# Performance work log

Hardware: AMD Instinct MI355X
Metric: run time of the kernel (lower is better)

## Reference

```python
import jax, jax.numpy as jnp
import numpy as np

B, C, T = 256, 9, 128
D, S, NL, EXP, DTR, DCONV = 24, 16, 4, 2, 2, 4
DI = EXP * D  # 48
STEMK, PK, PS = 5, 16, 4
NP = (T - PK) // PS + 1  # 29 patches
NCLS = 6


def setup_inputs() -> dict:
    key = jax.random.key(0)
    ks = iter(jax.random.split(key, 48))
    r = lambda shape, s=0.02: jax.random.normal(next(ks), shape, jnp.float32) * s
    return dict(
        x=jax.random.normal(next(ks), (B, T, C), jnp.float32),
        stem_w=r((D, 1, STEMK), 0.4),
        stem_bn_g=jnp.ones((D,)), stem_bn_b=jnp.zeros((D,)),
        stem_bn_m=jnp.zeros((D,)), stem_bn_v=jnp.ones((D,)),
        pd_w=r((D, 1, PK), 0.3),
        pp_w=r((D, D, 1), 0.3),
        patch_bn_g=jnp.ones((D,)), patch_bn_b=jnp.zeros((D,)),
        patch_bn_m=jnp.zeros((D,)), patch_bn_v=jnp.ones((D,)),
        pos_embed=r((1, NP, D)),
        ln1_g=jnp.ones((NL, D)), ln1_b=jnp.zeros((NL, D)),
        ln2_g=jnp.ones((NL, D)), ln2_b=jnp.zeros((NL, D)),
        in_w=r((NL, 2 * DI, D), 0.05),
        conv_w=r((NL, DI, 1, DCONV), 0.3), conv_b=jnp.zeros((NL, DI)),
        xproj_w=r((NL, DTR + 2 * S, DI), 0.05),
        dt_w=r((NL, DI, DTR), 0.1), dt_b=jnp.full((NL, DI), -2.0),
        A_log=jnp.log(jnp.broadcast_to(jnp.arange(1, S + 1, dtype=jnp.float32), (NL, DI, S))),
        Dp=jnp.ones((NL, DI)),
        out_w=r((NL, D, DI), 0.05),
        attn_w=r((D, D)), attn_b=jnp.zeros((D,)),
        ctx=r((D,)),
        head_g=jnp.ones((D,)), head_b=jnp.zeros((D,)),
        head_w=r((NCLS, D)), head_bias=jnp.zeros((NCLS,)),
    )


def _conv1d(x, w, stride, pad, groups=1):
    # x: [N, Cin, L], w: [Cout, Cin//groups, K]
    return jax.lax.conv_general_dilated(
        x, w, (stride,), [pad], dimension_numbers=('NCH', 'OIH', 'NCH'),
        feature_group_count=groups)


def _bn(x, g, b, m, v):  # eval-mode BatchNorm1d on [N, C, L]
    return (x - m[:, None]) * jax.lax.rsqrt(v[:, None] + 1e-5) * g[:, None] + b[:, None]


def _ln(x, g, b):
    mu = x.mean(-1, keepdims=True)
    var = ((x - mu) ** 2).mean(-1, keepdims=True)
    return (x - mu) * jax.lax.rsqrt(var + 1e-5) * g + b


def _selective_scan(u, dt, A, Bm, Cm):
    # u, dt: [N,L,DI]; A: [DI,S]; Bm, Cm: [N,L,S]
    dA = jnp.exp(dt[..., None] * A)                      # [N,L,DI,S]
    dBu = (dt * u)[..., None] * Bm[:, :, None, :]        # [N,L,DI,S]

    def step(h, inp):
        dA_t, dBu_t, C_t = inp
        h = dA_t * h + dBu_t                             # [N,DI,S]
        y = jnp.einsum('nds,ns->nd', h, C_t)
        return h, y

    h0 = jnp.zeros(dA.shape[:1] + dA.shape[2:], dA.dtype)
    _, ys = jax.lax.scan(step, h0, (dA.swapaxes(0, 1), dBu.swapaxes(0, 1), Cm.swapaxes(0, 1)))
    return ys.swapaxes(0, 1)                             # [N,L,DI]


def _mamba(x, in_w, conv_w, conv_b, xproj_w, dt_w, dt_b, A_log, Dp, out_w):
    # x: [N,L,D]
    xz = x @ in_w.T                                      # [N,L,2*DI]
    u, z = jnp.split(xz, 2, axis=-1)
    # causal depthwise conv (torch pads d_conv-1 both sides then truncates to L)
    uc = _conv1d(u.swapaxes(1, 2), conv_w, 1, (DCONV - 1, 0), groups=DI)
    uc = jax.nn.silu(uc + conv_b[None, :, None]).swapaxes(1, 2)   # [N,L,DI]
    dbl = uc @ xproj_w.T                                 # [N,L,DTR+2S]
    dtr, Bm, Cm = jnp.split(dbl, [DTR, DTR + S], axis=-1)
    dt = jax.nn.softplus(dtr @ dt_w.T + dt_b)            # [N,L,DI]
    A = -jnp.exp(A_log)                                  # [DI,S]
    y = _selective_scan(uc, dt, A, Bm, Cm) + uc * Dp
    y = y * jax.nn.silu(z)
    return y @ out_w.T                                   # [N,L,D]


def reference(x, stem_w, stem_bn_g, stem_bn_b, stem_bn_m, stem_bn_v,
              pd_w, pp_w, patch_bn_g, patch_bn_b, patch_bn_m, patch_bn_v,
              pos_embed, ln1_g, ln1_b, ln2_g, ln2_b,
              in_w, conv_w, conv_b, xproj_w, dt_w, dt_b, A_log, Dp, out_w,
              attn_w, attn_b, ctx, head_g, head_b, head_w, head_bias):
    Bsz = x.shape[0]
    # channel-independent reshape: [B,T,C] -> [B*C,1,T]
    h = x.transpose(0, 2, 1).reshape(Bsz * C, 1, T)
    # CI stem: shared single-channel conv + BN + SiLU
    h = _conv1d(h, stem_w, 1, (STEMK // 2, STEMK // 2))
    h = jax.nn.silu(_bn(h, stem_bn_g, stem_bn_b, stem_bn_m, stem_bn_v))  # [N,D,T]
    # patch embed: depthwise conv (k=16,s=4,pad=4,groups=D) + pointwise + BN
    h = _conv1d(h, pd_w, PS, (PK // 4, PK // 4), groups=D)
    h = _conv1d(h, pp_w, 1, (0, 0))
    h = _bn(h, patch_bn_g, patch_bn_b, patch_bn_m, patch_bn_v)
    h = h.swapaxes(1, 2)[:, :NP, :] + pos_embed          # [N,NP,D]
    # weight-tied bidirectional Mamba blocks
    for i in range(NL):
        res = h
        hn = _ln(h, ln1_g[i], ln1_b[i])
        args = (in_w[i], conv_w[i], conv_b[i], xproj_w[i], dt_w[i], dt_b[i], A_log[i], Dp[i], out_w[i])
        fwd = _mamba(hn, *args)
        bwd = jnp.flip(_mamba(jnp.flip(hn, axis=1), *args), axis=1)
        h = _ln(res + fwd + bwd, ln2_g[i], ln2_b[i])
    # gated temporal attention pooling
    u = jnp.tanh(h @ attn_w.T + attn_b)                  # [N,NP,D]
    alpha = jax.nn.softmax(jnp.einsum('nld,d->nl', u, ctx), axis=-1)
    c = jnp.einsum('nl,nld->nd', alpha, h)               # [N,D]
    # channel fusion: mean over sensor channels
    c = c.reshape(Bsz, C, D).mean(axis=1)                # [B,D]
    # head
    c = _ln(c, head_g, head_b)
    return c @ head_w.T + head_bias                      # [B,NCLS]
```

## Files before the change

### kernel.cpp

```cpp
#include <hip/hip_runtime.h>
#include <hip/hip_bf16.h>
#include <math.h>

#define B_    256
#define C_    9
#define T_    128
#define D_    24
#define S_    16
#define NL_   4
#define DI_   48
#define NP_   29
#define NSEQ  (B_ * C_)
#define NCLS_ 6

#define LOG2E 1.44269504088896f

#if __has_builtin(__builtin_amdgcn_exp2f)
#define EXP2F __builtin_amdgcn_exp2f
#else
#define EXP2F exp2f
#endif

__device__ __forceinline__ float fsilu(float x) {
    return __fdividef(x, 1.f + __expf(-x));
}

struct Params {
    const float *x;
    const float *stem_w, *stem_bn_g, *stem_bn_b, *stem_bn_m, *stem_bn_v;
    const float *pd_w, *pp_w, *patch_bn_g, *patch_bn_b, *patch_bn_m, *patch_bn_v;
    const float *pos_embed, *ln1_g, *ln1_b, *ln2_g, *ln2_b;
    const float *in_w, *conv_w, *conv_b, *xproj_w, *dt_w, *dt_b, *A_log, *Dp, *out_w;
    const float *attn_w, *attn_b, *ctx;
    float *cout;
};

__device__ __forceinline__ void ln_rows(const float* src, float* dst,
                                        const float* g, const float* bb, int tid) {
    int row = tid >> 3, sub = tid & 7;
    if (row < NP_) {
        const float* r = src + row * 24;
        float s = 0.f;
        for (int j = sub; j < 24; j += 8) s += r[j];
        s += __shfl_xor(s, 1); s += __shfl_xor(s, 2); s += __shfl_xor(s, 4);
        float mu = s * (1.f / 24.f);
        float v = 0.f;
        for (int j = sub; j < 24; j += 8) { float d0 = r[j] - mu; v = fmaf(d0, d0, v); }
        v += __shfl_xor(v, 1); v += __shfl_xor(v, 2); v += __shfl_xor(v, 4);
        float rs = rsqrtf(v * (1.f / 24.f) + 1e-5f);
        for (int j = sub; j < 24; j += 8) dst[row * 24 + j] = (r[j] - mu) * rs * g[j] + bb[j];
    }
}

#define OF_H    0
#define OF_HN   696
#define OF_U    1392
#define OF_Z    2784
#define OF_UCF  4176
#define OF_UCB  5568
#define OF_BCF  6960
#define OF_BCB  7888
#define OF_DTRF 8816
#define OF_DTRB 8874
#define SM_TOT  8932

__global__ __launch_bounds__(256, 4) void mamba_seq_kernel(Params P) {
    __shared__ float sm[SM_TOT];
    const int tid = threadIdx.x;
    const int n = blockIdx.x;
    const int b = n / C_, cch = n - b * C_;

    float* s_h    = sm + OF_H;
    float* s_hn   = sm + OF_HN;
    float* s_u    = sm + OF_U;
    float* s_z    = sm + OF_Z;
    float* s_ucf  = sm + OF_UCF;
    float* s_ucb  = sm + OF_UCB;
    float* s_bcf  = sm + OF_BCF;
    float* s_bcb  = sm + OF_BCB;
    float* s_dtrf = sm + OF_DTRF;
    float* s_dtrb = sm + OF_DTRB;

    float* xp  = sm + OF_UCF;
    float* h0p = sm + OF_UCF + 132;

    if (tid < 132) {
        float v = 0.f;
        int t = tid - 2;
        if (t >= 0 && t < T_) v = P.x[(b * T_ + t) * C_ + cch];
        xp[tid] = v;
    }
    for (int idx = tid; idx < 24 * 8; idx += 256) {
        int d = idx >> 3, j = idx & 7;
        h0p[d * 136 + (j < 4 ? j : j + 128)] = 0.f;
    }
    __syncthreads();
    for (int idx = tid; idx < 24 * 128; idx += 256) {
        int d = idx >> 7, t = idx & 127;
        const float* w = P.stem_w + d * 5;
        float acc = 0.f;
        #pragma unroll
        for (int k = 0; k < 5; k++) acc = fmaf(w[k], xp[t + k], acc);
        float sc = rsqrtf(P.stem_bn_v[d] + 1e-5f) * P.stem_bn_g[d];
        float val = (acc - P.stem_bn_m[d]) * sc + P.stem_bn_b[d];
        h0p[d * 136 + 4 + t] = fsilu(val);
    }
    __syncthreads();
    for (int idx = tid; idx < 24 * 31; idx += 256) {
        int d = idx / 31, l = idx - d * 31;
        const float* w = P.pd_w + d * 16;
        const float* src = h0p + d * 136 + l * 4;
        float acc = 0.f;
        #pragma unroll
        for (int k = 0; k < 16; k++) acc = fmaf(w[k], src[k], acc);
        s_u[idx] = acc;
    }
    __syncthreads();
    for (int idx = tid; idx < NP_ * 24; idx += 256) {
        int l = idx / 24, e = idx - l * 24;
        const float* w = P.pp_w + e * 24;
        float acc = 0.f;
        #pragma unroll
        for (int d = 0; d < 24; d++) acc = fmaf(w[d], s_u[d * 31 + l], acc);
        float sc = rsqrtf(P.patch_bn_v[e] + 1e-5f) * P.patch_bn_g[e];
        acc = (acc - P.patch_bn_m[e]) * sc + P.patch_bn_b[e];
        s_h[idx] = acc + P.pos_embed[idx];
    }
    __syncthreads();

    for (int il = 0; il < NL_; ++il) {
        const float* in_w_i   = P.in_w   + il * 96 * 24;
        const float* conv_w_i = P.conv_w + il * 48 * 4;
        const float* conv_b_i = P.conv_b + il * 48;
        const float* xpr_i    = P.xproj_w+ il * 34 * 48;
        const float* dt_w_i   = P.dt_w   + il * 48 * 2;
        const float* dt_b_i   = P.dt_b   + il * 48;
        const float* A_log_i  = P.A_log  + il * 48 * 16;
        const float* Dp_i     = P.Dp     + il * 48;
        const float* out_w_i  = P.out_w  + il * 24 * 48;

        ln_rows(s_h, s_hn, P.ln1_g + il * 24, P.ln1_b + il * 24, tid);
        __syncthreads();

        if (tid < 192) {
            int j  = tid >> 1;
            int l0 = (tid & 1) ? 15 : 0;
            int l1 = (tid & 1) ? NP_ : 15;
            const float4* w4 = (const float4*)(in_w_i + j * 24);
            float4 w0 = w4[0], w1 = w4[1], w2 = w4[2], w3 = w4[3], w4v = w4[4], w5 = w4[5];
            float* dst = (j < 48) ? (s_u + j) : (s_z + (j - 48));
            for (int l = l0; l < l1; ++l) {
                const float4* h4 = (const float4*)(s_hn + l * 24);
                float4 a0 = h4[0], a1 = h4[1], a2 = h4[2], a3 = h4[3], a4 = h4[4], a5 = h4[5];
                float acc;
                acc = a0.x * w0.x; acc = fmaf(a0.y, w0.y, acc); acc = fmaf(a0.z, w0.z, acc); acc = fmaf(a0.w, w0.w, acc);
                acc = fmaf(a1.x, w1.x, acc); acc = fmaf(a1.y, w1.y, acc); acc = fmaf(a1.z, w1.z, acc); acc = fmaf(a1.w, w1.w, acc);
                acc = fmaf(a2.x, w2.x, acc); acc = fmaf(a2.y, w2.y, acc); acc = fmaf(a2.z, w2.z, acc); acc = fmaf(a2.w, w2.w, acc);
                acc = fmaf(a3.x, w3.x, acc); acc = fmaf(a3.y, w3.y, acc); acc = fmaf(a3.z, w3.z, acc); acc = fmaf(a3.w, w3.w, acc);
                acc = fmaf(a4.x, w4v.x, acc); acc = fmaf(a4.y, w4v.y, acc); acc = fmaf(a4.z, w4v.z, acc); acc = fmaf(a4.w, w4v.w, acc);
                acc = fmaf(a5.x, w5.x, acc); acc = fmaf(a5.y, w5.y, acc); acc = fmaf(a5.z, w5.z, acc); acc = fmaf(a5.w, w5.w, acc);
                dst[l * 48] = acc;
            }
        }
        __syncthreads();

        for (int idx = tid; idx < NP_ * 48; idx += 256) {
            int l = idx / 48, d = idx - l * 48;
            const float* w = conv_w_i + d * 4;
            float w0 = w[0], w1 = w[1], w2 = w[2], w3 = w[3];
            float bb = conv_b_i[d];
            float accf = bb, accb = bb;
            if (l >= 3) accf = fmaf(w0, s_u[(l - 3) * 48 + d], accf);
            if (l >= 2) accf = fmaf(w1, s_u[(l - 2) * 48 + d], accf);
            if (l >= 1) accf = fmaf(w2, s_u[(l - 1) * 48 + d], accf);
            accf = fmaf(w3, s_u[l * 48 + d], accf);
            if (l + 3 < NP_) accb = fmaf(w0, s_u[(l + 3) * 48 + d], accb);
            if (l + 2 < NP_) accb = fmaf(w1, s_u[(l + 2) * 48 + d], accb);
            if (l + 1 < NP_) accb = fmaf(w2, s_u[(l + 1) * 48 + d], accb);
            accb = fmaf(w3, s_u[l * 48 + d], accb);
            s_ucf[idx] = fsilu(accf);
            s_ucb[idx] = fsilu(accb);
            s_z[idx] = fsilu(s_z[idx]);
        }
        __syncthreads();

        if (tid < 204) {
            int lg = tid / 68;
            int ch = tid - lg * 68;
            int l0 = lg * 10;
            int l1 = (lg == 2) ? NP_ : (l0 + 10);
            int dir = ch >= 34;
            int j = ch - (dir ? 34 : 0);
            const float* ucp = dir ? s_ucb : s_ucf;
            const float4* w4 = (const float4*)(xpr_i + j * 48);
            float4 w[12];
            #pragma unroll
            for (int q = 0; q < 12; q++) w[q] = w4[q];
            float* dst; int stride;
            if (j < 2) { dst = (dir ? s_dtrb : s_dtrf) + j; stride = 2; }
            else       { dst = (dir ? s_bcb  : s_bcf ) + (j - 2); stride = 32; }
            for (int l = l0; l < l1; ++l) {
                const float4* u4 = (const float4*)(ucp + l * 48);
                float acc = 0.f;
                #pragma unroll
                for (int q = 0; q < 12; q++) {
                    float4 a = u4[q];
                    acc = fmaf(a.x, w[q].x, fmaf(a.y, w[q].y, fmaf(a.z, w[q].z, fmaf(a.w, w[q].w, acc))));
                }
                dst[l * stride] = acc;
            }
        }
        __syncthreads();

        {
            int wv = tid >> 6, lane = tid & 63;
            if (wv < 2 && lane < 48) {
                const int d = lane;
                const float* dtr = wv ? s_dtrb : s_dtrf;
                float* ucio      = wv ? s_ucb  : s_ucf;
                const float* bc  = wv ? s_bcb  : s_bcf;
                float dtw0 = dt_w_i[d * 2], dtw1 = dt_w_i[d * 2 + 1], dtb = dt_b_i[d];
                float Dpd = Dp_i[d];
                float A2[16];
                bool alin = true;
                {
                    const float4* a4 = (const float4*)(A_log_i + d * 16);
                    #pragma unroll
                    for (int q = 0; q < 4; q++) {
                        float4 av = a4[q];
                        A2[4*q+0] = -__expf(av.x) * LOG2E;
                        A2[4*q+1] = -__expf(av.y) * LOG2E;
                        A2[4*q+2] = -__expf(av.z) * LOG2E;
                        A2[4*q+3] = -__expf(av.w) * LOG2E;
                    }
                    float a0c = A2[0];
                    #pragma unroll
                    for (int s = 1; s < 16; s++)
                        alin = alin && (fabsf(A2[s] - (s + 1) * a0c) <= 1e-4f * (s + 1) * fabsf(a0c));
                }
                float hs[16];
                #pragma unroll
                for (int s = 0; s < 16; s++) hs[s] = 0.f;

                if (alin) {
                    const float a0 = A2[0];
                    int l = wv ? (NP_ - 1) : 0;
                    float2 tt = *(const float2*)(dtr + l * 2);
                    float u_ld = ucio[l * 48 + d];
                    float draw = fmaf(tt.y, dtw1, fmaf(tt.x, dtw0, dtb));
                    float dtc = (draw > 15.f) ? draw : __logf(1.f + __expf(draw));
                    float dtu = dtc * u_ld;
                    float r1 = EXP2F(dtc * a0);
                    float r2 = r1 * r1, r4 = r2 * r2, r8 = r4 * r4;

                    for (int p = 0; p < NP_; p++) {
                        const int lc = l;
                        const float u_c = u_ld, dtu_c = dtu;
                        const float c1 = r1, c2 = r2, c4 = r4, c8 = r8;
                        if (p + 1 < NP_) {
                            l = wv ? (NP_ - 2 - p) : (p + 1);
                            tt = *(const float2*)(dtr + l * 2);
                            u_ld = ucio[l * 48 + d];
                            draw = fmaf(tt.y, dtw1, fmaf(tt.x, dtw0, dtb));
                            dtc = (draw > 15.f) ? draw : __logf(1.f + __expf(draw));
                            dtu = dtc * u_ld;
                            r1 = EXP2F(dtc * a0);
                            r2 = r1 * r1; r4 = r2 * r2; r8 = r4 * r4;
                        }
                        const float4* bcv = (const float4*)(bc + lc * 32);
                        float4 B0 = bcv[0], B1 = bcv[1], B2 = bcv[2], B3 = bcv[3];
                        float4 C0 = bcv[4], C1 = bcv[5], C2 = bcv[6], C3 = bcv[7];
                        float p3  = c2 * c1,  p5  = c4 * c1,  p6  = c4 * c2,  p7  = c4 * p3;
                        float p9  = c8 * c1,  p10 = c8 * c2,  p11 = c8 * p3,  p12 = c8 * c4;
                        float p13 = c8 * p5,  p14 = c8 * p6,  p15 = c8 * p7,  p16 = c8 * c8;
                        float y0 = 0.f, y1 = 0.f, y2 = 0.f, y3 = 0.f;
#define SFX(si, dA, Bc, Cc, ya) { hs[si] = fmaf(dA, hs[si], dtu_c * (Bc)); ya = fmaf(hs[si], (Cc), ya); }
                        SFX(0,  c1,  B0.x, C0.x, y0) SFX(1,  c2,  B0.y, C0.y, y1)
                        SFX(2,  p3,  B0.z, C0.z, y2) SFX(3,  c4,  B0.w, C0.w, y3)
                        SFX(4,  p5,  B1.x, C1.x, y0) SFX(5,  p6,  B1.y, C1.y, y1)
                        SFX(6,  p7,  B1.z, C1.z, y2) SFX(7,  c8,  B1.w, C1.w, y3)
                        SFX(8,  p9,  B2.x, C2.x, y0) SFX(9,  p10, B2.y, C2.y, y1)
                        SFX(10, p11, B2.z, C2.z, y2) SFX(11, p12, B2.w, C2.w, y3)
                        SFX(12, p13, B3.x, C3.x, y0) SFX(13, p14, B3.y, C3.y, y1)
                        SFX(14, p15, B3.z, C3.z, y2) SFX(15, p16, B3.w, C3.w, y3)
#undef SFX
                        float y = (y0 + y1) + (y2 + y3);
                        float v = fmaf(u_c, Dpd, y) * s_z[lc * 48 + d];
                        ucio[lc * 48 + d] = v;
                    }
                } else {
                    for (int p = 0; p < NP_; p++) {
                        int l = wv ? (NP_ - 1 - p) : p;
                        float2 tt = *(const float2*)(dtr + l * 2);
                        float draw = fmaf(tt.y, dtw1, fmaf(tt.x, dtw0, dtb));
                        float dtc = (draw > 15.f) ? draw : __logf(1.f + __expf(draw));
                        float u_ld = ucio[l * 48 + d];
                        float dtu = dtc * u_ld;
                        const float4* bcv = (const float4*)(bc + l * 32);
                        float4 B0 = bcv[0], B1 = bcv[1], B2 = bcv[2], B3 = bcv[3];
                        float4 C0 = bcv[4], C1 = bcv[5], C2 = bcv[6], C3 = bcv[7];
                        float y0 = 0.f, y1 = 0.f, y2 = 0.f, y3 = 0.f;
#define SGEN(si, Bc, Cc, ya) { float dA = EXP2F(dtc * A2[si]); hs[si] = fmaf(dA, hs[si], dtu * (Bc)); ya = fmaf(hs[si], (Cc), ya); }
                        SGEN(0,  B0.x, C0.x, y0) SGEN(1,  B0.y, C0.y, y1)
                        SGEN(2,  B0.z, C0.z, y2) SGEN(3,  B0.w, C0.w, y3)
                        SGEN(4,  B1.x, C1.x, y0) SGEN(5,  B1.y, C1.y, y1)
                        SGEN(6,  B1.z, C1.z, y2) SGEN(7,  B1.w, C1.w, y3)
                        SGEN(8,  B2.x, C2.x, y0) SGEN(9,  B2.y, C2.y, y1)
                        SGEN(10, B2.z, C2.z, y2) SGEN(11, B2.w, C2.w, y3)
                        SGEN(12, B3.x, C3.x, y0) SGEN(13, B3.y, C3.y, y1)
                        SGEN(14, B3.z, C3.z, y2) SGEN(15, B3.w, C3.w, y3)
#undef SGEN
                        float y = (y0 + y1) + (y2 + y3);
                        float v = fmaf(u_ld, Dpd, y) * s_z[l * 48 + d];
                        ucio[l * 48 + d] = v;
                    }
                }
            }
        }
        __syncthreads();

        if (tid < 192) {
            int e = tid >> 3, lg = tid & 7;
            const float4* w4 = (const float4*)(out_w_i + e * 48);
            float4 w[12];
            #pragma unroll
            for (int q = 0; q < 12; q++) w[q] = w4[q];
            for (int l = lg; l < NP_; l += 8) {
                const float4* f4 = (const float4*)(s_ucf + l * 48);
                const float4* b4 = (const float4*)(s_ucb + l * 48);
                float acc = s_h[l * 24 + e];
                #pragma unroll
                for (int q = 0; q < 12; q++) {
                    float4 af = f4[q], ab = b4[q];
                    float ax = af.x + ab.x, ay = af.y + ab.y, az = af.z + ab.z, aw = af.w + ab.w;
                    acc = fmaf(ax, w[q].x, fmaf(ay, w[q].y, fmaf(az, w[q].z, fmaf(aw, w[q].w, acc))));
                }
                s_hn[l * 24 + e] = acc;
            }
        }
        __syncthreads();

        ln_rows(s_hn, s_h, P.ln2_g + il * 24, P.ln2_b + il * 24, tid);
        __syncthreads();
    }

    for (int idx = tid; idx < NP_ * 24; idx += 256) {
        int l = idx / 24, d2 = idx - l * 24;
        const float* w = P.attn_w + d2 * 24;
        const float* hr = s_h + l * 24;
        float acc = P.attn_b[d2];
        #pragma unroll
        for (int e = 0; e < 24; e++) acc = fmaf(hr[e], w[e], acc);
        s_u[idx] = tanhf(acc) * P.ctx[d2];
    }
    __syncthreads();
    if (tid < NP_) {
        float s = 0.f;
        for (int d = 0; d < 24; d++) s += s_u[tid * 24 + d];
        s_dtrf[tid] = s;
    }
    __syncthreads();
    if (tid < 64) {
        float v = (tid < NP_) ? s_dtrf[tid] : -1e30f;
        float m = v;
        #pragma unroll
        for (int o = 32; o >= 1; o >>= 1) m = fmaxf(m, __shfl_xor(m, o));
        float e = (tid < NP_) ? __expf(v - m) : 0.f;
        float s = e;
        #pragma unroll
        for (int o = 32; o >= 1; o >>= 1) s += __shfl_xor(s, o);
        if (tid < NP_) s_dtrf[tid] = __fdividef(e, s);
    }
    __syncthreads();
    if (tid < 24) {
        float acc = 0.f;
        for (int l = 0; l < NP_; l++) acc = fmaf(s_dtrf[l], s_h[l * 24 + tid], acc);
        P.cout[n * 24 + tid] = acc;
    }
}

__global__ __launch_bounds__(64) void head_kernel(const float* __restrict__ cws,
                                                  const float* __restrict__ hg,
                                                  const float* __restrict__ hb,
                                                  const float* __restrict__ hw,
                                                  const float* __restrict__ hbias,
                                                  float* __restrict__ out) {
    __shared__ float sy[24];
    int bidx = blockIdx.x, t = threadIdx.x;
    float c = 0.f;
    if (t < 24) {
        float acc = 0.f;
        for (int j = 0; j < C_; j++) acc += cws[(bidx * C_ + j) * 24 + t];
        c = acc * (1.f / 9.f);
    }
    float s = (t < 24) ? c : 0.f;
    #pragma unroll
    for (int o = 32; o >= 1; o >>= 1) s += __shfl_xor(s, o);
    float mu = s * (1.f / 24.f);
    float dv = (t < 24) ? (c - mu) : 0.f;
    float q = dv * dv;
    #pragma unroll
    for (int o = 32; o >= 1; o >>= 1) q += __shfl_xor(q, o);
    float rs = rsqrtf(q * (1.f / 24.f) + 1e-5f);
    if (t < 24) sy[t] = dv * rs * hg[t] + hb[t];
    __syncthreads();
    if (t < NCLS_) {
        float acc = hbias[t];
        #pragma unroll
        for (int d = 0; d < 24; d++) acc = fmaf(sy[d], hw[t * 24 + d], acc);
        out[bidx * NCLS_ + t] = acc;
    }
}

extern "C" void kernel_launch(void* const* d_in, const int* in_sizes, int n_in,
                              void* d_out, int out_size, void* d_ws, size_t ws_size,
                              hipStream_t stream) {
    (void)in_sizes; (void)n_in; (void)out_size; (void)ws_size;
    Params P;
    P.x          = (const float*)d_in[0];
    P.stem_w     = (const float*)d_in[1];
    P.stem_bn_g  = (const float*)d_in[2];
    P.stem_bn_b  = (const float*)d_in[3];
    P.stem_bn_m  = (const float*)d_in[4];
    P.stem_bn_v  = (const float*)d_in[5];
    P.pd_w       = (const float*)d_in[6];
    P.pp_w       = (const float*)d_in[7];
    P.patch_bn_g = (const float*)d_in[8];
    P.patch_bn_b = (const float*)d_in[9];
    P.patch_bn_m = (const float*)d_in[10];
    P.patch_bn_v = (const float*)d_in[11];
    P.pos_embed  = (const float*)d_in[12];
    P.ln1_g      = (const float*)d_in[13];
    P.ln1_b      = (const float*)d_in[14];
    P.ln2_g      = (const float*)d_in[15];
    P.ln2_b      = (const float*)d_in[16];
    P.in_w       = (const float*)d_in[17];
    P.conv_w     = (const float*)d_in[18];
    P.conv_b     = (const float*)d_in[19];
    P.xproj_w    = (const float*)d_in[20];
    P.dt_w       = (const float*)d_in[21];
    P.dt_b       = (const float*)d_in[22];
    P.A_log      = (const float*)d_in[23];
    P.Dp         = (const float*)d_in[24];
    P.out_w      = (const float*)d_in[25];
    P.attn_w     = (const float*)d_in[26];
    P.attn_b     = (const float*)d_in[27];
    P.ctx        = (const float*)d_in[28];
    P.cout       = (float*)d_ws;

    mamba_seq_kernel<<<dim3(NSEQ), dim3(256), 0, stream>>>(P);
    head_kernel<<<dim3(B_), dim3(64), 0, stream>>>(
        (const float*)d_ws,
        (const float*)d_in[29],
        (const float*)d_in[30],
        (const float*)d_in[31],
        (const float*)d_in[32],
        (float*)d_out);
}
```

Measured before the change: 450.8 us.

## Split selective scan state across thread pairs and pad uc rows to 52

The selective scan now uses 192 threads instead of 96. Each (direction, channel) pair is handled by two lanes that each own 8 of the 16 state entries, and their partial outputs are combined with a shuffle. The uc buffers get a row stride of 52 instead of 48, which changes the LDS bank mapping. The goal is to shorten the serial scan's critical path and spread it over more wavefronts. The cost is duplicated dt/softplus/exp work per pair, extra shuffles, and a little more shared memory.

```diff
diff --git a/kernel.cpp b/kernel.cpp
--- a/kernel.cpp
+++ b/kernel.cpp
@@ -57,12 +57,12 @@
 #define OF_U    1392
 #define OF_Z    2784
 #define OF_UCF  4176
-#define OF_UCB  5568
-#define OF_BCF  6960
-#define OF_BCB  7888
-#define OF_DTRF 8816
-#define OF_DTRB 8874
-#define SM_TOT  8932
+#define OF_UCB  5684
+#define OF_BCF  7192
+#define OF_BCB  8120
+#define OF_DTRF 9048
+#define OF_DTRB 9106
+#define SM_TOT  9164
 
 __global__ __launch_bounds__(256, 4) void mamba_seq_kernel(Params P) {
     __shared__ float sm[SM_TOT];
@@ -178,8 +178,8 @@
             if (l + 2 < NP_) accb = fmaf(w1, s_u[(l + 2) * 48 + d], accb);
             if (l + 1 < NP_) accb = fmaf(w2, s_u[(l + 1) * 48 + d], accb);
             accb = fmaf(w3, s_u[l * 48 + d], accb);
-            s_ucf[idx] = fsilu(accf);
-            s_ucb[idx] = fsilu(accb);
+            s_ucf[l * 52 + d] = fsilu(accf);
+            s_ucb[l * 52 + d] = fsilu(accb);
             s_z[idx] = fsilu(s_z[idx]);
         }
         __syncthreads();
@@ -200,7 +200,7 @@
             if (j < 2) { dst = (dir ? s_dtrb : s_dtrf) + j; stride = 2; }
             else       { dst = (dir ? s_bcb  : s_bcf ) + (j - 2); stride = 32; }
             for (int l = l0; l < l1; ++l) {
-                const float4* u4 = (const float4*)(ucp + l * 48);
+                const float4* u4 = (const float4*)(ucp + l * 52);
                 float acc = 0.f;
                 #pragma unroll
                 for (int q = 0; q < 12; q++) {
@@ -212,108 +212,105 @@
         }
         __syncthreads();
 
-        {
-            int wv = tid >> 6, lane = tid & 63;
-            if (wv < 2 && lane < 48) {
-                const int d = lane;
-                const float* dtr = wv ? s_dtrb : s_dtrf;
-                float* ucio      = wv ? s_ucb  : s_ucf;
-                const float* bc  = wv ? s_bcb  : s_bcf;
-                float dtw0 = dt_w_i[d * 2], dtw1 = dt_w_i[d * 2 + 1], dtb = dt_b_i[d];
-                float Dpd = Dp_i[d];
-                float A2[16];
-                bool alin = true;
-                {
-                    const float4* a4 = (const float4*)(A_log_i + d * 16);
-                    #pragma unroll
-                    for (int q = 0; q < 4; q++) {
-                        float4 av = a4[q];
-                        A2[4*q+0] = -__expf(av.x) * LOG2E;
-                        A2[4*q+1] = -__expf(av.y) * LOG2E;
-                        A2[4*q+2] = -__expf(av.z) * LOG2E;
-                        A2[4*q+3] = -__expf(av.w) * LOG2E;
+        if (tid < 192) {
+            const int dir = tid >= 96;
+            const int rr  = tid - (dir ? 96 : 0);
+            const int d   = rr >> 1;
+            const int sh  = rr & 1;
+            const float* dtr = dir ? s_dtrb : s_dtrf;
+            float* ucio      = dir ? s_ucb  : s_ucf;
+            const float* bc  = dir ? s_bcb  : s_bcf;
+            const float dtw0 = dt_w_i[d * 2], dtw1 = dt_w_i[d * 2 + 1], dtb = dt_b_i[d];
+            const float Dpd = Dp_i[d];
+            float a0 = -__expf(A_log_i[d * 16]) * LOG2E;
+            bool alin = true;
+            #pragma unroll
+            for (int s = 1; s < 16; s++) {
+                float as = -__expf(A_log_i[d * 16 + s]) * LOG2E;
+                alin = alin && (fabsf(as - (s + 1) * a0) <= 1e-4f * (s + 1) * fabsf(a0));
+            }
+            float hs[8];
+            #pragma unroll
+            for (int s = 0; s < 8; s++) hs[s] = 0.f;
+
+            if (alin) {
+                int l = dir ? (NP_ - 1) : 0;
+                float2 tt = *(const float2*)(dtr + l * 2);
+                float u_ld = ucio[l * 52 + d];
+                float z_ld = s_z[l * 48 + d];
+                const float4* bv = (const float4*)(bc + l * 32);
+                float4 Bv0 = bv[2 * sh], Bv1 = bv[2 * sh + 1];
+                float4 Cv0 = bv[4 + 2 * sh], Cv1 = bv[5 + 2 * sh];
+                float draw = fmaf(tt.y, dtw1, fmaf(tt.x, dtw0, dtb));
+                float dtc = (draw > 15.f) ? draw : __logf(1.f + __expf(draw));
+                float dtu = dtc * u_ld;
+                float r1 = EXP2F(dtc * a0);
+
+                for (int p = 0; p < NP_; p++) {
+                    const int lc = p;
+                    (void)lc;
+                    const int lcur = l;
+                    const float u_c = u_ld, z_c = z_ld, dtu_c = dtu;
+                    const float4 Ba = Bv0, Bb = Bv1, Ca = Cv0, Cb = Cv1;
+                    float c2 = r1 * r1, c4 = c2 * c2, c8 = c4 * c4;
+                    float p3 = c2 * r1, p5 = c4 * r1, p6 = c4 * c2, p7 = c4 * p3;
+                    float qm = sh ? c8 : 1.0f;
+                    float dA0 = r1 * qm, dA1 = c2 * qm, dA2 = p3 * qm, dA3 = c4 * qm;
+                    float dA4 = p5 * qm, dA5 = p6 * qm, dA6 = p7 * qm, dA7 = c8 * qm;
+                    if (p + 1 < NP_) {
+                        l = dir ? (NP_ - 2 - p) : (p + 1);
+                        tt = *(const float2*)(dtr + l * 2);
+                        u_ld = ucio[l * 52 + d];
+                        z_ld = s_z[l * 48 + d];
+                        const float4* bn = (const float4*)(bc + l * 32);
+                        Bv0 = bn[2 * sh]; Bv1 = bn[2 * sh + 1];
+                        Cv0 = bn[4 + 2 * sh]; Cv1 = bn[5 + 2 * sh];
+                        draw = fmaf(tt.y, dtw1, fmaf(tt.x, dtw0, dtb));
+                        dtc = (draw > 15.f) ? draw : __logf(1.f + __expf(draw));
+                        dtu = dtc * u_ld;
+                        r1 = EXP2F(dtc * a0);
                     }
-                    float a0c = A2[0];
-                    #pragma unroll
-                    for (int s = 1; s < 16; s++)
-                        alin = alin && (fabsf(A2[s] - (s + 1) * a0c) <= 1e-4f * (s + 1) * fabsf(a0c));
+                    float y0, y1;
+                    hs[0] = fmaf(dA0, hs[0], dtu_c * Ba.x); y0 = hs[0] * Ca.x;
+                    hs[1] = fmaf(dA1, hs[1], dtu_c * Ba.y); y1 = hs[1] * Ca.y;
+                    hs[2] = fmaf(dA2, hs[2], dtu_c * Ba.z); y0 = fmaf(hs[2], Ca.z, y0);
+                    hs[3] = fmaf(dA3, hs[3], dtu_c * Ba.w); y1 = fmaf(hs[3], Ca.w, y1);
+                    hs[4] = fmaf(dA4, hs[4], dtu_c * Bb.x); y0 = fmaf(hs[4], Cb.x, y0);
+                    hs[5] = fmaf(dA5, hs[5], dtu_c * Bb.y); y1 = fmaf(hs[5], Cb.y, y1);
+                    hs[6] = fmaf(dA6, hs[6], dtu_c * Bb.z); y0 = fmaf(hs[6], Cb.z, y0);
+                    hs[7] = fmaf(dA7, hs[7], dtu_c * Bb.w); y1 = fmaf(hs[7], Cb.w, y1);
+                    float y = y0 + y1;
+                    y += __shfl_xor(y, 1);
+                    float v = fmaf(u_c, Dpd, y) * z_c;
+                    if (sh == 0) ucio[lcur * 52 + d] = v;
                 }
-                float hs[16];
-                #pragma unroll
-                for (int s = 0; s < 16; s++) hs[s] = 0.f;
-
-                if (alin) {
-                    const float a0 = A2[0];
-                    int l = wv ? (NP_ - 1) : 0;
+            } else {
+                for (int p = 0; p < NP_; p++) {
+                    int l = dir ? (NP_ - 1 - p) : p;
                     float2 tt = *(const float2*)(dtr + l * 2);
-                    float u_ld = ucio[l * 48 + d];
                     float draw = fmaf(tt.y, dtw1, fmaf(tt.x, dtw0, dtb));
                     float dtc = (draw > 15.f) ? draw : __logf(1.f + __expf(draw));
+                    float u_ld = ucio[l * 52 + d];
+                    float z_ld = s_z[l * 48 + d];
                     float dtu = dtc * u_ld;
-                    float r1 = EXP2F(dtc * a0);
-                    float r2 = r1 * r1, r4 = r2 * r2, r8 = r4 * r4;
-
-                    for (int p = 0; p < NP_; p++) {
-                        const int lc = l;
-                        const float u_c = u_ld, dtu_c = dtu;
-                        const float c1 = r1, c2 = r2, c4 = r4, c8 = r8;
-                        if (p + 1 < NP_) {
-                            l = wv ? (NP_ - 2 - p) : (p + 1);
-                            tt = *(const float2*)(dtr + l * 2);
-                            u_ld = ucio[l * 48 + d];
-                            draw = fmaf(tt.y, dtw1, fmaf(tt.x, dtw0, dtb));
-                            dtc = (draw > 15.f) ? draw : __logf(1.f + __expf(draw));
-                            dtu = dtc * u_ld;
-                            r1 = EXP2F(dtc * a0);
-                            r2 = r1 * r1; r4 = r2 * r2; r8 = r4 * r4;
-                        }
-                        const float4* bcv = (const float4*)(bc + lc * 32);
-                        float4 B0 = bcv[0], B1 = bcv[1], B2 = bcv[2], B3 = bcv[3];
-                        float4 C0 = bcv[4], C1 = bcv[5], C2 = bcv[6], C3 = bcv[7];
-                        float p3  = c2 * c1,  p5  = c4 * c1,  p6  = c4 * c2,  p7  = c4 * p3;
-                        float p9  = c8 * c1,  p10 = c8 * c2,  p11 = c8 * p3,  p12 = c8 * c4;
-                        float p13 = c8 * p5,  p14 = c8 * p6,  p15 = c8 * p7,  p16 = c8 * c8;
-                        float y0 = 0.f, y1 = 0.f, y2 = 0.f, y3 = 0.f;
-#define SFX(si, dA, Bc, Cc, ya) { hs[si] = fmaf(dA, hs[si], dtu_c * (Bc)); ya = fmaf(hs[si], (Cc), ya); }
-                        SFX(0,  c1,  B0.x, C0.x, y0) SFX(1,  c2,  B0.y, C0.y, y1)
-                        SFX(2,  p3,  B0.z, C0.z, y2) SFX(3,  c4,  B0.w, C0.w, y3)
-                        SFX(4,  p5,  B1.x, C1.x, y0) SFX(5,  p6,  B1.y, C1.y, y1)
-                        SFX(6,  p7,  B1.z, C1.z, y2) SFX(7,  c8,  B1.w, C1.w, y3)
-                        SFX(8,  p9,  B2.x, C2.x, y0) SFX(9,  p10, B2.y, C2.y, y1)
-                        SFX(10, p11, B2.z, C2.z, y2) SFX(11, p12, B2.w, C2.w, y3)
-                        SFX(12, p13, B3.x, C3.x, y0) SFX(13, p14, B3.y, C3.y, y1)
-                        SFX(14, p15, B3.z, C3.z, y2) SFX(15, p16, B3.w, C3.w, y3)
-#undef SFX
-                        float y = (y0 + y1) + (y2 + y3);
-                        float v = fmaf(u_c, Dpd, y) * s_z[lc * 48 + d];
-                        ucio[lc * 48 + d] = v;
+                    const float4* bv = (const float4*)(bc + l * 32);
+                    float4 Ba = bv[2 * sh], Bb = bv[2 * sh + 1];
+                    float4 Ca = bv[4 + 2 * sh], Cb = bv[5 + 2 * sh];
+                    float y0 = 0.f;
+                    #pragma unroll
+                    for (int i = 0; i < 8; i++) {
+                        float Bi = (i < 4) ? ((i == 0) ? Ba.x : (i == 1) ? Ba.y : (i == 2) ? Ba.z : Ba.w)
+                                           : ((i == 4) ? Bb.x : (i == 5) ? Bb.y : (i == 6) ? Bb.z : Bb.w);
+                        float Ci = (i < 4) ? ((i == 0) ? Ca.x : (i == 1) ? Ca.y : (i == 2) ? Ca.z : Ca.w)
+                                           : ((i == 4) ? Cb.x : (i == 5) ? Cb.y : (i == 6) ? Cb.z : Cb.w);
+                        float aa = -__expf(A_log_i[d * 16 + sh * 8 + i]) * LOG2E;
+                        float dA = EXP2F(dtc * aa);
+                        hs[i] = fmaf(dA, hs[i], dtu * Bi);
+                        y0 = fmaf(hs[i], Ci, y0);
                     }
-                } else {
-                    for (int p = 0; p < NP_; p++) {
-                        int l = wv ? (NP_ - 1 - p) : p;
-                        float2 tt = *(const float2*)(dtr + l * 2);
-                        float draw = fmaf(tt.y, dtw1, fmaf(tt.x, dtw0, dtb));
-                        float dtc = (draw > 15.f) ? draw : __logf(1.f + __expf(draw));
-                        float u_ld = ucio[l * 48 + d];
-                        float dtu = dtc * u_ld;
-                        const float4* bcv = (const float4*)(bc + l * 32);
-                        float4 B0 = bcv[0], B1 = bcv[1], B2 = bcv[2], B3 = bcv[3];
-                        float4 C0 = bcv[4], C1 = bcv[5], C2 = bcv[6], C3 = bcv[7];
-                        float y0 = 0.f, y1 = 0.f, y2 = 0.f, y3 = 0.f;
-#define SGEN(si, Bc, Cc, ya) { float dA = EXP2F(dtc * A2[si]); hs[si] = fmaf(dA, hs[si], dtu * (Bc)); ya = fmaf(hs[si], (Cc), ya); }
-                        SGEN(0,  B0.x, C0.x, y0) SGEN(1,  B0.y, C0.y, y1)
-                        SGEN(2,  B0.z, C0.z, y2) SGEN(3,  B0.w, C0.w, y3)
-                        SGEN(4,  B1.x, C1.x, y0) SGEN(5,  B1.y, C1.y, y1)
-                        SGEN(6,  B1.z, C1.z, y2) SGEN(7,  B1.w, C1.w, y3)
-                        SGEN(8,  B2.x, C2.x, y0) SGEN(9,  B2.y, C2.y, y1)
-                        SGEN(10, B2.z, C2.z, y2) SGEN(11, B2.w, C2.w, y3)
-                        SGEN(12, B3.x, C3.x, y0) SGEN(13, B3.y, C3.y, y1)
-                        SGEN(14, B3.z, C3.z, y2) SGEN(15, B3.w, C3.w, y3)
-#undef SGEN
-                        float y = (y0 + y1) + (y2 + y3);
-                        float v = fmaf(u_ld, Dpd, y) * s_z[l * 48 + d];
-                        ucio[l * 48 + d] = v;
-                    }
+                    float y = y0 + __shfl_xor(y0, 1);
+                    float v = fmaf(u_ld, Dpd, y) * z_ld;
+                    if (sh == 0) ucio[l * 52 + d] = v;
                 }
             }
         }
@@ -326,8 +323,8 @@
             #pragma unroll
             for (int q = 0; q < 12; q++) w[q] = w4[q];
             for (int l = lg; l < NP_; l += 8) {
-                const float4* f4 = (const float4*)(s_ucf + l * 48);
-                const float4* b4 = (const float4*)(s_ucb + l * 48);
+                const float4* f4 = (const float4*)(s_ucf + l * 52);
+                const float4* b4 = (const float4*)(s_ucb + l * 52);
                 float acc = s_h[l * 24 + e];
                 #pragma unroll
                 for (int q = 0; q < 12; q++) {
```

Result: faster. 424.0 us (-6.0%).
